# Optimization experiments

Measured on AMD Instinct MI355X. Metric: run time of the kernel, lower is better.

Reference implementation:

```python
import jax, jax.numpy as jnp
import numpy as np

N, T, F, T_dim, D = 256, 12, 32, 8, 64

def setup_inputs() -> dict:
    key = jax.random.key(0)
    ks = jax.random.split(key, 8)
    return {
        "x": jax.random.normal(ks[0], (N, T, F), jnp.float32),
        "Wq": jax.random.normal(ks[1], (N * T_dim, F, D), jnp.float32) * 0.1,
        "Wk": jax.random.normal(ks[2], (N * T_dim, F, D), jnp.float32) * 0.1,
        "Wv": jax.random.normal(ks[3], (N * T_dim, F, D), jnp.float32) * 0.1,
        "bq": jnp.zeros((N * T_dim, 1, D), jnp.float32),
        "bk": jnp.zeros((N * T_dim, 1, D), jnp.float32),
        "bv": jnp.zeros((N * T_dim, 1, D), jnp.float32),
        "w1": jax.random.normal(ks[4], (T_dim, T_dim * T * T), jnp.float32) * (2.0 / (T_dim * T * T)) ** 0.5,
        "b1": jnp.zeros((T_dim,), jnp.float32),
        "w2": jax.random.normal(ks[5], (1, T_dim), jnp.float32) * 0.5,
        "b2": jnp.zeros((1,), jnp.float32),
        "w3": jax.random.normal(ks[6], (D, D * T_dim), jnp.float32) * (2.0 / (D * T_dim)) ** 0.5,
        "b3": jnp.zeros((D,), jnp.float32),
        "w4": jax.random.normal(ks[7], (F, D), jnp.float32) * (2.0 / D) ** 0.5,
        "b4": jnp.zeros((F,), jnp.float32),
    }

def reference(x, Wq, Wk, Wv, bq, bk, bv, w1, b1, w2, b2, w3, b3, w4, b4):
    norm = 1.0 / np.sqrt(D).astype(np.float32)
    # mat_a: (N*T_dim, T, F) -- x broadcast across T_dim 'time scales'
    mat_a = jnp.broadcast_to(x[:, None], (N, T_dim, T, F)).reshape(-1, T, F)
    q = jnp.einsum('btf,bfd->btd', mat_a, Wq) + bq  # (N*T_dim, T, D)
    k = jnp.einsum('btf,bfd->btd', mat_a, Wk) + bk
    v = jnp.einsum('btf,bfd->btd', mat_a, Wv) + bv
    q4 = q.reshape(N, T_dim, T, D)
    k4 = k.reshape(N, T_dim, T, D)
    # pairwise scores: (N, N, T_dim, T, T)
    alpha = jnp.einsum('iktd,jksd->ijkts', q4, k4) * norm
    alpha = alpha.reshape(N, N, T_dim * T * T)
    h = jax.nn.relu(alpha @ w1.T + b1)            # (N, N, T_dim); dropout = identity (eval)
    s = (h @ w2.T + b2)[..., 0]                   # (N, N)
    att_score = jax.nn.softmax(s, axis=1)
    v4 = v.reshape(N, T_dim, T, D)
    b = jnp.einsum('ij,jktd->iktd', att_score, v4)   # (N, T_dim, T, D)
    b = b.transpose(0, 2, 3, 1).reshape(N, T, D * T_dim)
    y = jax.nn.relu(b @ w3.T + b3)                # (N, T, D); dropout = identity (eval)
    y = y @ w4.T + b4                             # (N, T, F)
    return (y, att_score)
```

## Files before the change

### kernel.cpp

```cpp
#include <hip/hip_runtime.h>
#include <hip/hip_bf16.h>

typedef unsigned short ushort_t;
typedef __bf16 bf16x8 __attribute__((ext_vector_type(8)));
typedef float f32x4 __attribute__((ext_vector_type(4)));
typedef ushort_t ushort8 __attribute__((ext_vector_type(8)));
typedef ushort_t ushort4v __attribute__((ext_vector_type(4)));

#define GLOAD16(gp, lp) \
    __builtin_amdgcn_global_load_lds((const __attribute__((address_space(1))) void*)(gp), \
                                     (__attribute__((address_space(3))) void*)(lp), 16, 0, 0)

__device__ __forceinline__ ushort_t bf16bits(float x) {
    __hip_bfloat16 h = __float2bfloat16(x);
    return *(ushort_t*)&h;
}
__device__ __forceinline__ float bf2f(ushort_t u) {
    unsigned v = (unsigned)u << 16;
    float f;
    __builtin_memcpy(&f, &v, 4);
    return f;
}

__global__ __launch_bounds__(256) void qkv_kernel(
    const float* __restrict__ x,
    const float* __restrict__ Wq, const float* __restrict__ Wk, const float* __restrict__ Wv,
    const float* __restrict__ bq, const float* __restrict__ bk, const float* __restrict__ bv,
    ushort_t* __restrict__ qhi, ushort_t* __restrict__ kbf, ushort_t* __restrict__ vbf)
{
    __shared__ float xs[4][12 * 36];
    int tid = threadIdx.x;
    int wid = tid >> 6, l = tid & 63;
    int gid = blockIdx.x * 4 + wid;
    int mat = gid >> 11, b = gid & 2047;
    int j = b >> 3;

    const float* W    = (mat == 0) ? Wq : (mat == 1) ? Wk : Wv;
    const float* bias = (mat == 0) ? bq : (mat == 1) ? bk : bv;
    ushort_t*    out  = (mat == 0) ? qhi : (mat == 1) ? kbf : vbf;
    float scale = (mat == 0) ? 0.125f : 1.0f;

    {
        const float4* xsrc = (const float4*)(x + (size_t)j * 384);
        float4 g0 = xsrc[l];
        int flat0 = l * 4;
        float* dst0 = &xs[wid][(flat0 >> 5) * 36 + (flat0 & 31)];
        dst0[0] = g0.x; dst0[1] = g0.y; dst0[2] = g0.z; dst0[3] = g0.w;
        if (l < 32) {
            float4 g1 = xsrc[64 + l];
            int flat1 = 256 + l * 4;
            float* dst1 = &xs[wid][(flat1 >> 5) * 36 + (flat1 & 31)];
            dst1[0] = g1.x; dst1[1] = g1.y; dst1[2] = g1.z; dst1[3] = g1.w;
        }
    }
    __syncthreads();

    int dq = l & 15, tg = l >> 4;
    const f32x4* w4 = (const f32x4*)(W + (size_t)b * 2048);
    f32x4 a0 = {0.f,0.f,0.f,0.f}, a1 = a0, a2 = a0;
    const float* xr = &xs[wid][tg * 3 * 36];
    #pragma unroll
    for (int f4 = 0; f4 < 8; ++f4) {
        f32x4 w0 = w4[(f4 * 4 + 0) * 16 + dq];
        f32x4 w1_ = w4[(f4 * 4 + 1) * 16 + dq];
        f32x4 w2_ = w4[(f4 * 4 + 2) * 16 + dq];
        f32x4 w3_ = w4[(f4 * 4 + 3) * 16 + dq];
        float4 xa = *(const float4*)&xr[0 * 36 + f4 * 4];
        float4 xb = *(const float4*)&xr[1 * 36 + f4 * 4];
        float4 xc = *(const float4*)&xr[2 * 36 + f4 * 4];
        a0 += w0 * xa.x + w1_ * xa.y + w2_ * xa.z + w3_ * xa.w;
        a1 += w0 * xb.x + w1_ * xb.y + w2_ * xb.z + w3_ * xb.w;
        a2 += w0 * xc.x + w1_ * xc.y + w2_ * xc.z + w3_ * xc.w;
    }

    f32x4 bv4 = *(const f32x4*)(bias + (size_t)b * 64 + dq * 4);
    size_t obase = (size_t)b * 768 + dq * 4;
    f32x4 r;
    ushort4v u;
    r = (a0 + bv4) * scale;
    u[0] = bf16bits(r[0]); u[1] = bf16bits(r[1]); u[2] = bf16bits(r[2]); u[3] = bf16bits(r[3]);
    *(ushort4v*)(out + obase + (size_t)(tg * 3 + 0) * 64) = u;
    r = (a1 + bv4) * scale;
    u[0] = bf16bits(r[0]); u[1] = bf16bits(r[1]); u[2] = bf16bits(r[2]); u[3] = bf16bits(r[3]);
    *(ushort4v*)(out + obase + (size_t)(tg * 3 + 1) * 64) = u;
    r = (a2 + bv4) * scale;
    u[0] = bf16bits(r[0]); u[1] = bf16bits(r[1]); u[2] = bf16bits(r[2]); u[3] = bf16bits(r[3]);
    *(ushort4v*)(out + obase + (size_t)(tg * 3 + 2) * 64) = u;
}

__global__ __launch_bounds__(256, 2) void hgemm_kernel(
    const ushort_t* __restrict__ qhi, const ushort_t* __restrict__ kbf,
    const float* __restrict__ w1, ushort_t* __restrict__ hpart,
    const ushort_t* __restrict__ vbf, const float* __restrict__ w3, const float* __restrict__ w4,
    ushort_t* __restrict__ vt, float* __restrict__ w3t, float* __restrict__ w4t)
{
    __shared__ alignas(16) char sb[77056];
    int tid = threadIdx.x;
    int bid = blockIdx.x;

    if (bid >= 512) {
        if (bid < 896) {
            ushort_t (*ts)[264] = (ushort_t(*)[264])sb;
            int c0 = (bid - 512) * 16;
            int cc = tid & 15, jg = tid >> 4;
            #pragma unroll 4
            for (int jj = 0; jj < 16; ++jj) {
                int jx = jg * 16 + jj;
                ts[cc][jx] = vbf[(size_t)jx * 6144 + c0 + cc];
            }
            __syncthreads();
            #pragma unroll
            for (int c = 0; c < 16; ++c)
                vt[(size_t)(c0 + c) * 256 + tid] = ts[c][tid];
            return;
        }
        if (bid < 912) {
            int wb = bid - 896;
            #pragma unroll
            for (int r = 0; r < 8; ++r) {
                int e = wb * 2048 + r * 256 + tid;
                int dout = e >> 9, c3 = e & 511;
                int cb = ((c3 & 7) << 6) | (c3 >> 3);
                w3t[cb * 64 + dout] = w3[e];
            }
            return;
        }
        #pragma unroll
        for (int r = 0; r < 8; ++r) {
            int e = r * 256 + tid; int f = e >> 6, dd = e & 63;
            w4t[dd * 32 + f] = w4[e];
        }
        return;
    }

    ushort_t* Bs  = (ushort_t*)sb;
    ushort_t* As  = (ushort_t*)(sb + 65536);
    float*    w1s = (float*)(sb + 74752);

    int lane = tid & 63, wv = tid >> 6;
    int xcd = bid & 7, kq = bid >> 3;
    int z = xcd + 8 * (kq >> 5);
    int rem = kq & 31;
    int n0 = rem * 64, jb = rem * 8;
    int kk = z >> 1, thalf = (z & 1) * 6;
    ushort_t* Hout = hpart + (size_t)z * 524288;

    int j_loc = tid >> 5, d8 = (tid >> 2) & 7, mg = tid & 3;

    if (tid < 144) {
        int m = tid / 18, r = tid % 18;
        GLOAD16(w1 + (size_t)m * 1152 + kk * 144 + thalf * 12 + r * 4, &w1s[m * 72 + r * 4]);
    }
    ushort8 kreg[12];
    {
        const ushort_t* kp = kbf + (size_t)((jb + j_loc) * 8 + kk) * 768 + d8 * 8;
        #pragma unroll
        for (int s = 0; s < 12; ++s) kreg[s] = *(const ushort8*)(kp + s * 64);
    }
    __syncthreads();

    f32x4 acc[4][4] = {};

    #define GBUILD(st)                                                          \
    {                                                                           \
        float ag0[8] = {0.f,0.f,0.f,0.f,0.f,0.f,0.f,0.f};                       \
        float ag1[8] = {0.f,0.f,0.f,0.f,0.f,0.f,0.f,0.f};                       \
        _Pragma("unroll")                                                       \
        for (int s = 0; s < 12; ++s) {                                          \
            float kf[8];                                                        \
            _Pragma("unroll")                                                   \
            for (int dd = 0; dd < 8; ++dd) kf[dd] = bf2f(kreg[s][dd]);          \
            float wa = w1s[(mg * 2 + 0) * 72 + (st) * 12 + s];                  \
            float wb = w1s[(mg * 2 + 1) * 72 + (st) * 12 + s];                  \
            _Pragma("unroll")                                                   \
            for (int dd = 0; dd < 8; ++dd) {                                    \
                ag0[dd] += wa * kf[dd];                                         \
                ag1[dd] += wb * kf[dd];                                         \
            }                                                                   \
        }                                                                       \
        int row0 = j_loc * 8 + mg * 2;                                          \
        int sl0 = d8 ^ (row0 & 7), sl1 = d8 ^ ((row0 + 1) & 7);                 \
        ushort8 u0, u1;                                                         \
        _Pragma("unroll")                                                       \
        for (int dd = 0; dd < 8; ++dd) { u0[dd] = bf16bits(ag0[dd]); u1[dd] = bf16bits(ag1[dd]); } \
        *(ushort8*)&As[row0 * 72 + sl0 * 8] = u0;                               \
        *(ushort8*)&As[(row0 + 1) * 72 + sl1 * 8] = u1;                         \
    }

    #define STAGE_B(buf, st)                                                    \
    {                                                                           \
        int koff = kk * 768 + (thalf + (st)) * 64;                              \
        _Pragma("unroll")                                                       \
        for (int r = 0; r < 8; ++r) {                                           \
            int c = r * 256 + tid; int row = c >> 3, slot = c & 7;              \
            GLOAD16(qhi + (size_t)row * 6144 + koff + ((slot ^ (row & 7)) * 8), \
                    &Bs[(buf) * 16384 + c * 8]);                                \
        }                                                                       \
    }

    GBUILD(0);
    STAGE_B(0, 0);
    int cur = 0;
    for (int st = 0; st < 6; ++st) {
        __syncthreads();
        bf16x8 a[2][4], b[2][4];
        #pragma unroll
        for (int kh = 0; kh < 2; ++kh)
            #pragma unroll
            for (int mi = 0; mi < 4; ++mi) {
                int row = mi * 16 + (lane & 15);
                int slot = (kh * 4 + (lane >> 4)) ^ (row & 7);
                a[kh][mi] = *(const bf16x8*)&As[row * 72 + slot * 8];
            }
        #pragma unroll
        for (int kh = 0; kh < 2; ++kh)
            #pragma unroll
            for (int ni = 0; ni < 4; ++ni) {
                int row = wv * 64 + ni * 16 + (lane & 15);
                int slot = (kh * 4 + (lane >> 4)) ^ (row & 7);
                b[kh][ni] = *(const bf16x8*)&Bs[cur * 16384 + row * 64 + slot * 8];
            }
        __syncthreads();
        if (st + 1 < 6) { GBUILD(st + 1); STAGE_B(cur ^ 1, st + 1); }
        #pragma unroll
        for (int kh = 0; kh < 2; ++kh)
            #pragma unroll
            for (int mi = 0; mi < 4; ++mi)
                #pragma unroll
                for (int ni = 0; ni < 4; ++ni)
                    acc[mi][ni] = __builtin_amdgcn_mfma_f32_16x16x32_bf16(a[kh][mi], b[kh][ni], acc[mi][ni], 0, 0, 0);
        cur ^= 1;
    }
    #undef GBUILD
    #undef STAGE_B

    int r4 = (lane >> 4) * 4, cn = lane & 15;
    #pragma unroll
    for (int mi = 0; mi < 4; ++mi)
        #pragma unroll
        for (int ni = 0; ni < 4; ++ni) {
            int i = wv * 64 + ni * 16 + cn;
            int nb = n0 + mi * 16 + r4;
            ushort4v u;
            #pragma unroll
            for (int r = 0; r < 4; ++r) u[r] = bf16bits(acc[mi][ni][r]);
            *(ushort4v*)(Hout + (size_t)i * 2048 + nb) = u;
        }
}

__global__ __launch_bounds__(256) void score_softmax_kernel(
    const ushort_t* __restrict__ hpart, const float* __restrict__ b1g,
    const float* __restrict__ w2g, const float* __restrict__ b2g,
    float* __restrict__ att, ushort_t* __restrict__ attbf)
{
    int i = blockIdx.x, j = threadIdx.x;
    float hm[8];
    #pragma unroll
    for (int m = 0; m < 8; ++m) hm[m] = b1g[m];
    #pragma unroll 4
    for (int z = 0; z < 16; ++z) {
        ushort8 u = *(const ushort8*)(hpart + (size_t)z * 524288 + (size_t)i * 2048 + j * 8);
        #pragma unroll
        for (int m = 0; m < 8; ++m) hm[m] += bf2f(u[m]);
    }
    float sv = b2g[0];
    #pragma unroll
    for (int m = 0; m < 8; ++m) sv += fmaxf(hm[m], 0.f) * w2g[m];

    __shared__ float wred[4], wred2[4];
    float mx = sv;
    #pragma unroll
    for (int off = 32; off > 0; off >>= 1) mx = fmaxf(mx, __shfl_down(mx, off, 64));
    if ((j & 63) == 0) wred[j >> 6] = mx;
    __syncthreads();
    mx = fmaxf(fmaxf(wred[0], wred[1]), fmaxf(wred[2], wred[3]));

    float e = expf(sv - mx);
    float sum = e;
    #pragma unroll
    for (int off = 32; off > 0; off >>= 1) sum += __shfl_down(sum, off, 64);
    if ((j & 63) == 0) wred2[j >> 6] = sum;
    __syncthreads();
    sum = wred2[0] + wred2[1] + wred2[2] + wred2[3];

    float pv = e / sum;
    att[(size_t)i * 256 + j] = pv;
    attbf[(size_t)i * 256 + j] = bf16bits(pv);
}

__global__ __launch_bounds__(256) void av_kernel(
    const ushort_t* __restrict__ attbf, const ushort_t* __restrict__ vt,
    float* __restrict__ bmat)
{
    __shared__ ushort_t As[2][64 * 64];
    __shared__ ushort_t Bs[2][64 * 64];

    int tid = threadIdx.x, lane = tid & 63, wid = tid >> 6;
    int wr = wid >> 1, wc = wid & 1;
    int c0 = blockIdx.x * 64, i0 = blockIdx.y * 64;

    f32x4 acc[2][2] = {};

    #define STAGEAV(buf, koff)                                                              \
    {                                                                                       \
        _Pragma("unroll")                                                                   \
        for (int r = 0; r < 2; ++r) {                                                       \
            int c = r * 256 + tid; int row = c >> 3, slot = c & 7;                          \
            int so = (koff) + ((slot ^ (row & 7)) * 8);                                     \
            GLOAD16(vt + (size_t)(c0 + row) * 256 + so, &As[buf][c * 8]);                   \
            GLOAD16(attbf + (size_t)(i0 + row) * 256 + so, &Bs[buf][c * 8]);                \
        }                                                                                   \
    }

    int cur = 0;
    STAGEAV(0, 0);
    for (int s = 0; s < 4; ++s) {
        __syncthreads();
        if (s < 3) STAGEAV(cur ^ 1, (s + 1) * 64);
        #pragma unroll
        for (int kh = 0; kh < 2; ++kh) {
            bf16x8 a[2], b[2];
            #pragma unroll
            for (int mi = 0; mi < 2; ++mi) {
                int row = wr * 32 + mi * 16 + (lane & 15);
                int slot = (kh * 4 + (lane >> 4)) ^ (row & 7);
                a[mi] = *(const bf16x8*)&As[cur][row * 64 + slot * 8];
            }
            #pragma unroll
            for (int ni = 0; ni < 2; ++ni) {
                int row = wc * 32 + ni * 16 + (lane & 15);
                int slot = (kh * 4 + (lane >> 4)) ^ (row & 7);
                b[ni] = *(const bf16x8*)&Bs[cur][row * 64 + slot * 8];
            }
            #pragma unroll
            for (int mi = 0; mi < 2; ++mi)
                #pragma unroll
                for (int ni = 0; ni < 2; ++ni)
                    acc[mi][ni] = __builtin_amdgcn_mfma_f32_16x16x32_bf16(a[mi], b[ni], acc[mi][ni], 0, 0, 0);
        }
        cur ^= 1;
    }
    #undef STAGEAV

    int r4 = (lane >> 4) * 4, cn = lane & 15;
    #pragma unroll
    for (int mi = 0; mi < 2; ++mi)
        #pragma unroll
        for (int ni = 0; ni < 2; ++ni) {
            int i = i0 + wc * 32 + ni * 16 + cn;
            int c = c0 + wr * 32 + mi * 16 + r4;
            int kk = c / 768, rem = c - kk * 768;
            int t = rem >> 6, d = rem & 63;
            float4 val;
            val.x = acc[mi][ni][0]; val.y = acc[mi][ni][1];
            val.z = acc[mi][ni][2]; val.w = acc[mi][ni][3];
            *(float4*)(bmat + ((size_t)i * 12 + t) * 512 + kk * 64 + d) = val;
        }
}

__global__ __launch_bounds__(256) void out_kernel(
    const float* __restrict__ bmat, const float* __restrict__ w3t, const float* __restrict__ b3,
    const float* __restrict__ w4t, const float* __restrict__ b4, float* __restrict__ yout)
{
    int rb = blockIdx.x * 8;
    int tid = threadIdx.x;
    __shared__ float rows[8 * 512];
    __shared__ float y1s[8 * 64];
    const float4* src = (const float4*)(bmat + (size_t)rb * 512);
    #pragma unroll
    for (int r = 0; r < 4; ++r) ((float4*)rows)[tid + r * 256] = src[tid + r * 256];
    __syncthreads();

    int dout = tid & 63, rg = tid >> 6;
    float acc[2];
    float b3v = b3[dout];
    acc[0] = b3v; acc[1] = b3v;
    for (int c4 = 0; c4 < 128; ++c4) {
        float w0 = w3t[(c4 * 4 + 0) * 64 + dout];
        float w1v = w3t[(c4 * 4 + 1) * 64 + dout];
        float w2v = w3t[(c4 * 4 + 2) * 64 + dout];
        float w3v = w3t[(c4 * 4 + 3) * 64 + dout];
        #pragma unroll
        for (int jj = 0; jj < 2; ++jj) {
            float4 rv = *(const float4*)&rows[(rg * 2 + jj) * 512 + c4 * 4];
            acc[jj] += rv.x * w0 + rv.y * w1v + rv.z * w2v + rv.w * w3v;
        }
    }
    #pragma unroll
    for (int jj = 0; jj < 2; ++jj) y1s[(rg * 2 + jj) * 64 + dout] = fmaxf(acc[jj], 0.f);
    __syncthreads();

    int f = tid & 31, rh = tid >> 5;
    float a2 = b4[f];
    #pragma unroll
    for (int dd = 0; dd < 64; ++dd) a2 += y1s[rh * 64 + dd] * w4t[dd * 32 + f];
    yout[(size_t)(rb + rh) * 32 + f] = a2;
}

extern "C" void kernel_launch(void* const* d_in, const int* in_sizes, int n_in,
                              void* d_out, int out_size, void* d_ws, size_t ws_size,
                              hipStream_t stream) {
    (void)in_sizes; (void)n_in; (void)out_size; (void)ws_size;
    const float* x  = (const float*)d_in[0];
    const float* Wq = (const float*)d_in[1];
    const float* Wk = (const float*)d_in[2];
    const float* Wv = (const float*)d_in[3];
    const float* bq = (const float*)d_in[4];
    const float* bk = (const float*)d_in[5];
    const float* bv = (const float*)d_in[6];
    const float* w1 = (const float*)d_in[7];
    const float* b1 = (const float*)d_in[8];
    const float* w2 = (const float*)d_in[9];
    const float* b2 = (const float*)d_in[10];
    const float* w3 = (const float*)d_in[11];
    const float* b3 = (const float*)d_in[12];
    const float* w4 = (const float*)d_in[13];
    const float* b4 = (const float*)d_in[14];

    float* ws = (float*)d_ws;
    ushort_t* hpart = (ushort_t*)ws;
    size_t    off   = 4194304;
    ushort_t* qhi   = (ushort_t*)(ws + off);
    ushort_t* kbf   = (ushort_t*)(ws + off + 786432);
    ushort_t* vbf   = (ushort_t*)(ws + off + 1572864);
    ushort_t* vt    = (ushort_t*)(ws + off + 2359296);
    ushort_t* attbf = (ushort_t*)(ws + off + 3145728);
    float*    w3t   = ws + off + 3178496;
    float*    w4t   = ws + off + 3211264;
    float*    bmat  = ws + off + 3213312;

    float* yout = (float*)d_out;
    float* att  = (float*)d_out + 98304;

    qkv_kernel<<<1536, 256, 0, stream>>>(x, Wq, Wk, Wv, bq, bk, bv, qhi, kbf, vbf);
    hgemm_kernel<<<913, 256, 0, stream>>>(qhi, kbf, w1, hpart, vbf, w3, w4, vt, w3t, w4t);
    score_softmax_kernel<<<256, 256, 0, stream>>>(hpart, b1, w2, b2, att, attbf);
    av_kernel<<<dim3(96, 4), 256, 0, stream>>>(attbf, vt, bmat);
    out_kernel<<<384, 256, 0, stream>>>(bmat, w3t, b3, w4t, b4, yout);
}
```

Baseline: 62.11 us.

## Fuse softmax, AV and output stages into one cooperative kernel; halve hgemm tiles

Three tail kernels (score softmax, attention-times-V GEMM, output MLP) are merged into one cooperative kernel of 384 blocks that separates phases with grid-wide syncs. This removes two kernel launches and their gaps. The h-GEMM tile is also halved along the i dimension (128 instead of 256 rows), doubling its block count and cutting LDS use so three blocks can fit per CU. The trade-offs are grid.sync overhead, idle blocks during the softmax phase, and more redundant A-side building in the h-GEMM.

```diff
diff --git a/kernel.cpp b/kernel.cpp
--- a/kernel.cpp
+++ b/kernel.cpp
@@ -1,5 +1,8 @@
 #include <hip/hip_runtime.h>
 #include <hip/hip_bf16.h>
+#include <hip/hip_cooperative_groups.h>
+
+namespace cg = cooperative_groups;
 
 typedef unsigned short ushort_t;
 typedef __bf16 bf16x8 __attribute__((ext_vector_type(8)));
@@ -88,20 +91,20 @@
     *(ushort4v*)(out + obase + (size_t)(tg * 3 + 2) * 64) = u;
 }
 
-__global__ __launch_bounds__(256, 2) void hgemm_kernel(
+__global__ __launch_bounds__(256, 3) void hgemm_kernel(
     const ushort_t* __restrict__ qhi, const ushort_t* __restrict__ kbf,
     const float* __restrict__ w1, ushort_t* __restrict__ hpart,
     const ushort_t* __restrict__ vbf, const float* __restrict__ w3, const float* __restrict__ w4,
     ushort_t* __restrict__ vt, float* __restrict__ w3t, float* __restrict__ w4t)
 {
-    __shared__ alignas(16) char sb[77056];
+    __shared__ alignas(16) char sb[44288];
     int tid = threadIdx.x;
     int bid = blockIdx.x;
 
-    if (bid >= 512) {
-        if (bid < 896) {
+    if (bid >= 1024) {
+        if (bid < 1408) {
             ushort_t (*ts)[264] = (ushort_t(*)[264])sb;
-            int c0 = (bid - 512) * 16;
+            int c0 = (bid - 1024) * 16;
             int cc = tid & 15, jg = tid >> 4;
             #pragma unroll 4
             for (int jj = 0; jj < 16; ++jj) {
@@ -114,8 +117,8 @@
                 vt[(size_t)(c0 + c) * 256 + tid] = ts[c][tid];
             return;
         }
-        if (bid < 912) {
-            int wb = bid - 896;
+        if (bid < 1424) {
+            int wb = bid - 1408;
             #pragma unroll
             for (int r = 0; r < 8; ++r) {
                 int e = wb * 2048 + r * 256 + tid;
@@ -134,14 +137,15 @@
     }
 
     ushort_t* Bs  = (ushort_t*)sb;
-    ushort_t* As  = (ushort_t*)(sb + 65536);
-    float*    w1s = (float*)(sb + 74752);
+    ushort_t* As  = (ushort_t*)(sb + 32768);
+    float*    w1s = (float*)(sb + 41984);
 
     int lane = tid & 63, wv = tid >> 6;
     int xcd = bid & 7, kq = bid >> 3;
-    int z = xcd + 8 * (kq >> 5);
-    int rem = kq & 31;
-    int n0 = rem * 64, jb = rem * 8;
+    int z = xcd + 8 * (kq >> 6);
+    int rem = kq & 63;
+    int ntile = rem >> 1, itile = rem & 1;
+    int n0 = ntile * 64, i0 = itile * 128, jb = ntile * 8;
     int kk = z >> 1, thalf = (z & 1) * 6;
     ushort_t* Hout = hpart + (size_t)z * 524288;
 
@@ -159,7 +163,7 @@
     }
     __syncthreads();
 
-    f32x4 acc[4][4] = {};
+    f32x4 acc[4][2] = {};
 
     #define GBUILD(st)                                                          \
     {                                                                           \
@@ -191,10 +195,10 @@
     {                                                                           \
         int koff = kk * 768 + (thalf + (st)) * 64;                              \
         _Pragma("unroll")                                                       \
-        for (int r = 0; r < 8; ++r) {                                           \
+        for (int r = 0; r < 4; ++r) {                                           \
             int c = r * 256 + tid; int row = c >> 3, slot = c & 7;              \
-            GLOAD16(qhi + (size_t)row * 6144 + koff + ((slot ^ (row & 7)) * 8), \
-                    &Bs[(buf) * 16384 + c * 8]);                                \
+            GLOAD16(qhi + (size_t)(i0 + row) * 6144 + koff + ((slot ^ (row & 7)) * 8), \
+                    &Bs[(buf) * 8192 + c * 8]);                                 \
         }                                                                       \
     }
 
@@ -203,7 +207,7 @@
     int cur = 0;
     for (int st = 0; st < 6; ++st) {
         __syncthreads();
-        bf16x8 a[2][4], b[2][4];
+        bf16x8 a[2][4], b[2][2];
         #pragma unroll
         for (int kh = 0; kh < 2; ++kh)
             #pragma unroll
@@ -215,10 +219,10 @@
         #pragma unroll
         for (int kh = 0; kh < 2; ++kh)
             #pragma unroll
-            for (int ni = 0; ni < 4; ++ni) {
-                int row = wv * 64 + ni * 16 + (lane & 15);
+            for (int ni = 0; ni < 2; ++ni) {
+                int row = wv * 32 + ni * 16 + (lane & 15);
                 int slot = (kh * 4 + (lane >> 4)) ^ (row & 7);
-                b[kh][ni] = *(const bf16x8*)&Bs[cur * 16384 + row * 64 + slot * 8];
+                b[kh][ni] = *(const bf16x8*)&Bs[cur * 8192 + row * 64 + slot * 8];
             }
         __syncthreads();
         if (st + 1 < 6) { GBUILD(st + 1); STAGE_B(cur ^ 1, st + 1); }
@@ -227,7 +231,7 @@
             #pragma unroll
             for (int mi = 0; mi < 4; ++mi)
                 #pragma unroll
-                for (int ni = 0; ni < 4; ++ni)
+                for (int ni = 0; ni < 2; ++ni)
                     acc[mi][ni] = __builtin_amdgcn_mfma_f32_16x16x32_bf16(a[kh][mi], b[kh][ni], acc[mi][ni], 0, 0, 0);
         cur ^= 1;
     }
@@ -238,8 +242,8 @@
     #pragma unroll
     for (int mi = 0; mi < 4; ++mi)
         #pragma unroll
-        for (int ni = 0; ni < 4; ++ni) {
-            int i = wv * 64 + ni * 16 + cn;
+        for (int ni = 0; ni < 2; ++ni) {
+            int i = i0 + wv * 32 + ni * 16 + cn;
             int nb = n0 + mi * 16 + r4;
             ushort4v u;
             #pragma unroll
@@ -248,153 +252,159 @@
         }
 }
 
-__global__ __launch_bounds__(256) void score_softmax_kernel(
+__global__ __launch_bounds__(256) void tail_kernel(
     const ushort_t* __restrict__ hpart, const float* __restrict__ b1g,
     const float* __restrict__ w2g, const float* __restrict__ b2g,
-    float* __restrict__ att, ushort_t* __restrict__ attbf)
+    float* __restrict__ att, ushort_t* __restrict__ attbf,
+    const ushort_t* __restrict__ vt, float* __restrict__ bmat,
+    const float* __restrict__ w3t, const float* __restrict__ b3,
+    const float* __restrict__ w4t, const float* __restrict__ b4,
+    float* __restrict__ yout)
 {
-    int i = blockIdx.x, j = threadIdx.x;
-    float hm[8];
-    #pragma unroll
-    for (int m = 0; m < 8; ++m) hm[m] = b1g[m];
-    #pragma unroll 4
-    for (int z = 0; z < 16; ++z) {
-        ushort8 u = *(const ushort8*)(hpart + (size_t)z * 524288 + (size_t)i * 2048 + j * 8);
-        #pragma unroll
-        for (int m = 0; m < 8; ++m) hm[m] += bf2f(u[m]);
-    }
-    float sv = b2g[0];
-    #pragma unroll
-    for (int m = 0; m < 8; ++m) sv += fmaxf(hm[m], 0.f) * w2g[m];
-
-    __shared__ float wred[4], wred2[4];
-    float mx = sv;
-    #pragma unroll
-    for (int off = 32; off > 0; off >>= 1) mx = fmaxf(mx, __shfl_down(mx, off, 64));
-    if ((j & 63) == 0) wred[j >> 6] = mx;
-    __syncthreads();
-    mx = fmaxf(fmaxf(wred[0], wred[1]), fmaxf(wred[2], wred[3]));
-
-    float e = expf(sv - mx);
-    float sum = e;
-    #pragma unroll
-    for (int off = 32; off > 0; off >>= 1) sum += __shfl_down(sum, off, 64);
-    if ((j & 63) == 0) wred2[j >> 6] = sum;
-    __syncthreads();
-    sum = wred2[0] + wred2[1] + wred2[2] + wred2[3];
-
-    float pv = e / sum;
-    att[(size_t)i * 256 + j] = pv;
-    attbf[(size_t)i * 256 + j] = bf16bits(pv);
-}
-
-__global__ __launch_bounds__(256) void av_kernel(
-    const ushort_t* __restrict__ attbf, const ushort_t* __restrict__ vt,
-    float* __restrict__ bmat)
-{
-    __shared__ ushort_t As[2][64 * 64];
-    __shared__ ushort_t Bs[2][64 * 64];
-
-    int tid = threadIdx.x, lane = tid & 63, wid = tid >> 6;
-    int wr = wid >> 1, wc = wid & 1;
-    int c0 = blockIdx.x * 64, i0 = blockIdx.y * 64;
-
-    f32x4 acc[2][2] = {};
-
-    #define STAGEAV(buf, koff)                                                              \
-    {                                                                                       \
-        _Pragma("unroll")                                                                   \
-        for (int r = 0; r < 2; ++r) {                                                       \
-            int c = r * 256 + tid; int row = c >> 3, slot = c & 7;                          \
-            int so = (koff) + ((slot ^ (row & 7)) * 8);                                     \
-            GLOAD16(vt + (size_t)(c0 + row) * 256 + so, &As[buf][c * 8]);                   \
-            GLOAD16(attbf + (size_t)(i0 + row) * 256 + so, &Bs[buf][c * 8]);                \
-        }                                                                                   \
-    }
-
-    int cur = 0;
-    STAGEAV(0, 0);
-    for (int s = 0; s < 4; ++s) {
-        __syncthreads();
-        if (s < 3) STAGEAV(cur ^ 1, (s + 1) * 64);
-        #pragma unroll
-        for (int kh = 0; kh < 2; ++kh) {
-            bf16x8 a[2], b[2];
-            #pragma unroll
-            for (int mi = 0; mi < 2; ++mi) {
-                int row = wr * 32 + mi * 16 + (lane & 15);
-                int slot = (kh * 4 + (lane >> 4)) ^ (row & 7);
-                a[mi] = *(const bf16x8*)&As[cur][row * 64 + slot * 8];
-            }
+    cg::grid_group grid = cg::this_grid();
+    __shared__ alignas(16) char sb[33024];
+    int bid = blockIdx.x, tid = threadIdx.x;
+
+    if (bid < 256) {
+        int i = bid, j = tid;
+        float hm[8];
+        #pragma unroll
+        for (int m = 0; m < 8; ++m) hm[m] = b1g[m];
+        #pragma unroll 4
+        for (int z = 0; z < 16; ++z) {
+            ushort8 u = *(const ushort8*)(hpart + (size_t)z * 524288 + (size_t)i * 2048 + j * 8);
+            #pragma unroll
+            for (int m = 0; m < 8; ++m) hm[m] += bf2f(u[m]);
+        }
+        float sv = b2g[0];
+        #pragma unroll
+        for (int m = 0; m < 8; ++m) sv += fmaxf(hm[m], 0.f) * w2g[m];
+
+        float* wred  = (float*)sb;
+        float* wred2 = (float*)sb + 4;
+        float mx = sv;
+        #pragma unroll
+        for (int off = 32; off > 0; off >>= 1) mx = fmaxf(mx, __shfl_down(mx, off, 64));
+        if ((j & 63) == 0) wred[j >> 6] = mx;
+        __syncthreads();
+        mx = fmaxf(fmaxf(wred[0], wred[1]), fmaxf(wred[2], wred[3]));
+
+        float e = expf(sv - mx);
+        float sum = e;
+        #pragma unroll
+        for (int off = 32; off > 0; off >>= 1) sum += __shfl_down(sum, off, 64);
+        if ((j & 63) == 0) wred2[j >> 6] = sum;
+        __syncthreads();
+        sum = wred2[0] + wred2[1] + wred2[2] + wred2[3];
+
+        float pv = e / sum;
+        att[(size_t)i * 256 + j] = pv;
+        attbf[(size_t)i * 256 + j] = bf16bits(pv);
+    }
+    grid.sync();
+
+    {
+        ushort_t* As = (ushort_t*)sb;
+        ushort_t* Bs = (ushort_t*)(sb + 16384);
+        int bx = bid % 96, by = bid / 96;
+        int c0 = bx * 64, i0 = by * 64;
+        int lane = tid & 63, wid = tid >> 6;
+        int wr = wid >> 1, wc = wid & 1;
+
+        f32x4 acc[2][2] = {};
+
+        #define STAGEAV(buf, koff)                                                          \
+        {                                                                                   \
+            _Pragma("unroll")                                                               \
+            for (int r = 0; r < 2; ++r) {                                                   \
+                int c = r * 256 + tid; int row = c >> 3, slot = c & 7;                      \
+                int so = (koff) + ((slot ^ (row & 7)) * 8);                                 \
+                GLOAD16(vt + (size_t)(c0 + row) * 256 + so, &As[(buf) * 4096 + c * 8]);     \
+                GLOAD16(attbf + (size_t)(i0 + row) * 256 + so, &Bs[(buf) * 4096 + c * 8]);  \
+            }                                                                               \
+        }
+
+        int cur = 0;
+        STAGEAV(0, 0);
+        for (int s = 0; s < 4; ++s) {
+            __syncthreads();
+            if (s < 3) STAGEAV(cur ^ 1, (s + 1) * 64);
+            #pragma unroll
+            for (int kh = 0; kh < 2; ++kh) {
+                bf16x8 a[2], b[2];
+                #pragma unroll
+                for (int mi = 0; mi < 2; ++mi) {
+                    int row = wr * 32 + mi * 16 + (lane & 15);
+                    int slot = (kh * 4 + (lane >> 4)) ^ (row & 7);
+                    a[mi] = *(const bf16x8*)&As[cur * 4096 + row * 64 + slot * 8];
+                }
+                #pragma unroll
+                for (int ni = 0; ni < 2; ++ni) {
+                    int row = wc * 32 + ni * 16 + (lane & 15);
+                    int slot = (kh * 4 + (lane >> 4)) ^ (row & 7);
+                    b[ni] = *(const bf16x8*)&Bs[cur * 4096 + row * 64 + slot * 8];
+                }
+                #pragma unroll
+                for (int mi = 0; mi < 2; ++mi)
+                    #pragma unroll
+                    for (int ni = 0; ni < 2; ++ni)
+                        acc[mi][ni] = __builtin_amdgcn_mfma_f32_16x16x32_bf16(a[mi], b[ni], acc[mi][ni], 0, 0, 0);
+            }
+            cur ^= 1;
+        }
+        #undef STAGEAV
+
+        int r4 = (lane >> 4) * 4, cn = lane & 15;
+        #pragma unroll
+        for (int mi = 0; mi < 2; ++mi)
             #pragma unroll
             for (int ni = 0; ni < 2; ++ni) {
-                int row = wc * 32 + ni * 16 + (lane & 15);
-                int slot = (kh * 4 + (lane >> 4)) ^ (row & 7);
-                b[ni] = *(const bf16x8*)&Bs[cur][row * 64 + slot * 8];
-            }
-            #pragma unroll
-            for (int mi = 0; mi < 2; ++mi)
-                #pragma unroll
-                for (int ni = 0; ni < 2; ++ni)
-                    acc[mi][ni] = __builtin_amdgcn_mfma_f32_16x16x32_bf16(a[mi], b[ni], acc[mi][ni], 0, 0, 0);
-        }
-        cur ^= 1;
-    }
-    #undef STAGEAV
-
-    int r4 = (lane >> 4) * 4, cn = lane & 15;
-    #pragma unroll
-    for (int mi = 0; mi < 2; ++mi)
-        #pragma unroll
-        for (int ni = 0; ni < 2; ++ni) {
-            int i = i0 + wc * 32 + ni * 16 + cn;
-            int c = c0 + wr * 32 + mi * 16 + r4;
-            int kk = c / 768, rem = c - kk * 768;
-            int t = rem >> 6, d = rem & 63;
-            float4 val;
-            val.x = acc[mi][ni][0]; val.y = acc[mi][ni][1];
-            val.z = acc[mi][ni][2]; val.w = acc[mi][ni][3];
-            *(float4*)(bmat + ((size_t)i * 12 + t) * 512 + kk * 64 + d) = val;
-        }
-}
-
-__global__ __launch_bounds__(256) void out_kernel(
-    const float* __restrict__ bmat, const float* __restrict__ w3t, const float* __restrict__ b3,
-    const float* __restrict__ w4t, const float* __restrict__ b4, float* __restrict__ yout)
-{
-    int rb = blockIdx.x * 8;
-    int tid = threadIdx.x;
-    __shared__ float rows[8 * 512];
-    __shared__ float y1s[8 * 64];
-    const float4* src = (const float4*)(bmat + (size_t)rb * 512);
-    #pragma unroll
-    for (int r = 0; r < 4; ++r) ((float4*)rows)[tid + r * 256] = src[tid + r * 256];
-    __syncthreads();
-
-    int dout = tid & 63, rg = tid >> 6;
-    float acc[2];
-    float b3v = b3[dout];
-    acc[0] = b3v; acc[1] = b3v;
-    for (int c4 = 0; c4 < 128; ++c4) {
-        float w0 = w3t[(c4 * 4 + 0) * 64 + dout];
-        float w1v = w3t[(c4 * 4 + 1) * 64 + dout];
-        float w2v = w3t[(c4 * 4 + 2) * 64 + dout];
-        float w3v = w3t[(c4 * 4 + 3) * 64 + dout];
-        #pragma unroll
-        for (int jj = 0; jj < 2; ++jj) {
-            float4 rv = *(const float4*)&rows[(rg * 2 + jj) * 512 + c4 * 4];
-            acc[jj] += rv.x * w0 + rv.y * w1v + rv.z * w2v + rv.w * w3v;
-        }
-    }
-    #pragma unroll
-    for (int jj = 0; jj < 2; ++jj) y1s[(rg * 2 + jj) * 64 + dout] = fmaxf(acc[jj], 0.f);
-    __syncthreads();
-
-    int f = tid & 31, rh = tid >> 5;
-    float a2 = b4[f];
-    #pragma unroll
-    for (int dd = 0; dd < 64; ++dd) a2 += y1s[rh * 64 + dd] * w4t[dd * 32 + f];
-    yout[(size_t)(rb + rh) * 32 + f] = a2;
+                int i = i0 + wc * 32 + ni * 16 + cn;
+                int c = c0 + wr * 32 + mi * 16 + r4;
+                int kk = c / 768, rem = c - kk * 768;
+                int t = rem >> 6, d = rem & 63;
+                float4 val;
+                val.x = acc[mi][ni][0]; val.y = acc[mi][ni][1];
+                val.z = acc[mi][ni][2]; val.w = acc[mi][ni][3];
+                *(float4*)(bmat + ((size_t)i * 12 + t) * 512 + kk * 64 + d) = val;
+            }
+    }
+    grid.sync();
+
+    {
+        float* rows = (float*)sb;
+        float* y1s  = (float*)(sb + 16384);
+        int rb = bid * 8;
+        const float4* src = (const float4*)(bmat + (size_t)rb * 512);
+        #pragma unroll
+        for (int r = 0; r < 4; ++r) ((float4*)rows)[tid + r * 256] = src[tid + r * 256];
+        __syncthreads();
+
+        int dout = tid & 63, rg = tid >> 6;
+        float acc2[2];
+        float b3v = b3[dout];
+        acc2[0] = b3v; acc2[1] = b3v;
+        for (int c4 = 0; c4 < 128; ++c4) {
+            float w0 = w3t[(c4 * 4 + 0) * 64 + dout];
+            float w1v = w3t[(c4 * 4 + 1) * 64 + dout];
+            float w2v = w3t[(c4 * 4 + 2) * 64 + dout];
+            float w3v = w3t[(c4 * 4 + 3) * 64 + dout];
+            #pragma unroll
+            for (int jj = 0; jj < 2; ++jj) {
+                float4 rv = *(const float4*)&rows[(rg * 2 + jj) * 512 + c4 * 4];
+                acc2[jj] += rv.x * w0 + rv.y * w1v + rv.z * w2v + rv.w * w3v;
+            }
+        }
+        #pragma unroll
+        for (int jj = 0; jj < 2; ++jj) y1s[(rg * 2 + jj) * 64 + dout] = fmaxf(acc2[jj], 0.f);
+        __syncthreads();
+
+        int f = tid & 31, rh = tid >> 5;
+        float a2 = b4[f];
+        #pragma unroll
+        for (int dd = 0; dd < 64; ++dd) a2 += y1s[rh * 64 + dd] * w4t[dd * 32 + f];
+        yout[(size_t)(rb + rh) * 32 + f] = a2;
+    }
 }
 
 extern "C" void kernel_launch(void* const* d_in, const int* in_sizes, int n_in,
@@ -433,8 +443,10 @@
     float* att  = (float*)d_out + 98304;
 
     qkv_kernel<<<1536, 256, 0, stream>>>(x, Wq, Wk, Wv, bq, bk, bv, qhi, kbf, vbf);
-    hgemm_kernel<<<913, 256, 0, stream>>>(qhi, kbf, w1, hpart, vbf, w3, w4, vt, w3t, w4t);
-    score_softmax_kernel<<<256, 256, 0, stream>>>(hpart, b1, w2, b2, att, attbf);
-    av_kernel<<<dim3(96, 4), 256, 0, stream>>>(attbf, vt, bmat);
-    out_kernel<<<384, 256, 0, stream>>>(bmat, w3t, b3, w4t, b4, yout);
-}
+    hgemm_kernel<<<1425, 256, 0, stream>>>(qhi, kbf, w1, hpart, vbf, w3, w4, vt, w3t, w4t);
+
+    void* targs[] = { (void*)&hpart, (void*)&b1, (void*)&w2, (void*)&b2,
+                      (void*)&att, (void*)&attbf, (void*)&vt, (void*)&bmat,
+                      (void*)&w3t, (void*)&b3, (void*)&w4t, (void*)&b4, (void*)&yout };
+    hipLaunchCooperativeKernel((const void*)tail_kernel, dim3(384), dim3(256), targs, 0, stream);
+}
```

After: 175.6 us. +182.8%, slower.
